# Performance work log

Measured on AMD Instinct MI355X. Metric: run time of the kernel, lower is better.

Reference implementation:

```python
import jax, jax.numpy as jnp
import numpy as np

N, F, H, C, K = 4096, 128, 128, 10, 4  # nodes, feat dim, hidden, classes, num_graphs
EDGE_P = 0.005


def setup_inputs() -> dict:
    key = jax.random.key(0)
    ks = jax.random.split(key, 20)
    feat_matrix = jax.random.normal(ks[0], (N, F), jnp.float32)
    # binary adjacency (dense_to_sparse + GCNConv without edge_weight => weights all 1)
    adj = (jax.random.uniform(ks[1], (N, N, K)) < EDGE_P).astype(jnp.float32)
    adj_matrix = adj * (1.0 - jnp.eye(N, dtype=jnp.float32))[:, :, None]  # no self loops in input
    s = 0.05
    gcn_w1 = jax.random.normal(ks[2], (K, F, H), jnp.float32) * s
    gcn_b1 = jnp.zeros((K, H), jnp.float32)
    gcn_w2 = jax.random.normal(ks[3], (K, H, H), jnp.float32) * s
    gcn_b2 = jnp.zeros((K, H), jnp.float32)
    # PyTorch LSTM params (gate order i,f,g,o), forward and backward directions
    wih_f = jax.random.normal(ks[4], (4 * H, H), jnp.float32) * s
    whh_f = jax.random.normal(ks[5], (4 * H, H), jnp.float32) * s
    bih_f = jnp.zeros((4 * H,), jnp.float32)
    bhh_f = jnp.zeros((4 * H,), jnp.float32)
    wih_b = jax.random.normal(ks[6], (4 * H, H), jnp.float32) * s
    whh_b = jax.random.normal(ks[7], (4 * H, H), jnp.float32) * s
    bih_b = jnp.zeros((4 * H,), jnp.float32)
    bhh_b = jnp.zeros((4 * H,), jnp.float32)
    rnn_out_w = jax.random.normal(ks[8], (1, 2 * H), jnp.float32) * s
    rnn_out_b = jnp.zeros((1,), jnp.float32)
    out_w = jax.random.normal(ks[9], (C, H), jnp.float32) * s
    out_b = jnp.zeros((C,), jnp.float32)
    get_item_index = jnp.arange(N, dtype=jnp.int64)
    set_index = jax.random.randint(ks[10], (1024,), 0, N).astype(jnp.int64)
    val_index = jax.random.randint(ks[11], (1024,), 0, N).astype(jnp.int64)
    mask_matrix = jnp.ones((N,), jnp.bool_)
    return dict(feat_matrix=feat_matrix, adj_matrix=adj_matrix,
                gcn_w1=gcn_w1, gcn_b1=gcn_b1, gcn_w2=gcn_w2, gcn_b2=gcn_b2,
                wih_f=wih_f, whh_f=whh_f, bih_f=bih_f, bhh_f=bhh_f,
                wih_b=wih_b, whh_b=whh_b, bih_b=bih_b, bhh_b=bhh_b,
                rnn_out_w=rnn_out_w, rnn_out_b=rnn_out_b, out_w=out_w, out_b=out_b,
                get_item_index=get_item_index, set_index=set_index,
                val_index=val_index, mask_matrix=mask_matrix)


def _gcn_norm(adj):
    # GCNConv default: A_hat = A + I, sym-normalized D^-1/2 A_hat D^-1/2
    a_hat = adj + jnp.eye(adj.shape[0], dtype=adj.dtype)
    dinv = jax.lax.rsqrt(a_hat.sum(axis=1))
    return dinv[:, None] * a_hat * dinv[None, :]


def _lstm_dir(xs, wih, whh, bih, bhh, reverse):
    # xs: [N, K, H] -> hs: [N, K, H]; scan over the (short) block axis K
    n, h = xs.shape[0], whh.shape[1]
    def step(carry, x_t):
        hp, cp = carry
        g = x_t @ wih.T + hp @ whh.T + (bih + bhh)
        i, f, gg, o = jnp.split(g, 4, axis=-1)
        c = jax.nn.sigmoid(f) * cp + jax.nn.sigmoid(i) * jnp.tanh(gg)
        hn = jax.nn.sigmoid(o) * jnp.tanh(c)
        return (hn, c), hn
    init = (jnp.zeros((n, h), xs.dtype), jnp.zeros((n, h), xs.dtype))
    _, hs = jax.lax.scan(step, init, jnp.swapaxes(xs, 0, 1), reverse=reverse)
    return jnp.swapaxes(hs, 0, 1)


def reference(feat_matrix, adj_matrix, gcn_w1, gcn_b1, gcn_w2, gcn_b2,
              wih_f, whh_f, bih_f, bhh_f, wih_b, whh_b, bih_b, bhh_b,
              rnn_out_w, rnn_out_b, out_w, out_b,
              get_item_index, set_index, val_index, mask_matrix):
    k_blocks = adj_matrix.shape[-1]
    gnn_output = []
    for k in range(k_blocks):  # fixed small number of structurally distinct graph blocks
        an = _gcn_norm(adj_matrix[:, :, k])                 # [N, N]
        h = an @ (feat_matrix @ gcn_w1[k]) + gcn_b1[k]      # GCNConv 1 (no activation)
        h = an @ (h @ gcn_w2[k]) + gcn_b2[k]                # GCNConv 2
        gnn_output.append(h)
    gnn_out = jnp.stack(gnn_output, axis=1)                 # [N, K, H]
    h_fwd = _lstm_dir(gnn_out, wih_f, whh_f, bih_f, bhh_f, reverse=False)
    h_bwd = _lstm_dir(gnn_out, wih_b, whh_b, bih_b, bhh_b, reverse=True)
    rnn_hid = jnp.concatenate([h_fwd, h_bwd], axis=-1)      # [N, K, 2H]
    attn = jax.nn.softmax(rnn_hid @ rnn_out_w.T + rnn_out_b, axis=1)  # [N, K, 1]
    pooled = (gnn_out * attn).sum(axis=1)                   # [N, H]
    return jax.nn.softmax(pooled @ out_w.T + out_b, axis=-1)  # [N, C]
```

## Files before the change

### kernel.cpp

```cpp
#include <hip/hip_runtime.h>
#include <hip/hip_bf16.h>

#define NN 4096
#define HD 128
#define KG 4
#define NC 10
#define CAP 64

typedef __attribute__((ext_vector_type(8))) short bf16x8;
typedef __attribute__((ext_vector_type(4))) float f32x4;

__device__ inline unsigned short f2b(float x) {
    unsigned u = __float_as_uint(x);
    return (unsigned short)((u + 0x7FFFu + ((u >> 16) & 1u)) >> 16);
}
__device__ inline float b2f(unsigned short b) {
    return __uint_as_float((unsigned)b << 16);
}

__global__ __launch_bounds__(256) void setup_kernel(
    const float* __restrict__ adj, const float* __restrict__ feat,
    const float* __restrict__ wih_f, const float* __restrict__ whh_f,
    const float* __restrict__ bih_f, const float* __restrict__ bhh_f,
    const float* __restrict__ wih_b, const float* __restrict__ whh_b,
    const float* __restrict__ bih_b, const float* __restrict__ bhh_b,
    const float* __restrict__ gw1, const float* __restrict__ gw2,
    float* __restrict__ dinv, int* __restrict__ ecnt,
    unsigned short* __restrict__ edges, unsigned* __restrict__ featb,
    unsigned short* __restrict__ Wp, float* __restrict__ bp,
    unsigned short* __restrict__ Wg1p, unsigned short* __restrict__ Wg2p)
{
    int b = blockIdx.x;
    __shared__ int cnt[KG];
    if (b < NN) {
        int i = b;
        int lane = threadIdx.x & 63;
        if (threadIdx.x < KG) cnt[threadIdx.x] = 0;
        __syncthreads();
        const float4* row = (const float4*)(adj + (size_t)i * NN * KG);
        unsigned long long below = (1ull << lane) - 1ull;
        for (int j = threadIdx.x; j < NN; j += 256) {
            float4 v = row[j];
#pragma unroll
            for (int k = 0; k < KG; ++k) {
                float comp = (k == 0) ? v.x : (k == 1) ? v.y : (k == 2) ? v.z : v.w;
                unsigned long long mask = __ballot(comp != 0.f);
                if (mask) {
                    int base;
                    if (lane == 0) base = atomicAdd(&cnt[k], __popcll(mask));
                    base = __shfl(base, 0);
                    if (comp != 0.f) {
                        int p = base + (int)__popcll(mask & below);
                        if (p < CAP)
                            edges[((size_t)(k * NN + i)) * CAP + p] = (unsigned short)j;
                    }
                }
            }
        }
        __syncthreads();
        if (threadIdx.x < KG) {
            int c = cnt[threadIdx.x];
            ecnt[threadIdx.x * NN + i] = c > CAP ? CAP : c;
            dinv[threadIdx.x * NN + i] = rsqrtf((float)c + 1.0f);
        }
    } else if (b < NN + 1024) {
        int t = (b - NN) * 256 + threadIdx.x;
        int dir = t >> 17, rem = t & 131071;
        int n = rem >> 8, k = rem & 255;
        int hq = n >> 6, g = (n >> 4) & 3, hr = n & 15;
        int row = g * HD + hq * 16 + hr;
        const float* wih = dir ? wih_b : wih_f;
        const float* whh = dir ? whh_b : whh_f;
        Wp[t] = f2b(k < HD ? wih[row * HD + k] : whh[row * HD + (k - HD)]);
    } else if (b < NN + 1280) {
        int t = (b - NN - 1024) * 256 + threadIdx.x;
        int n = t >> 7, k = t & 127;
        Wg1p[t] = f2b(gw1[(((size_t)(n >> 7)) * HD + k) * HD + (n & 127)]);
    } else if (b < NN + 1536) {
        int t = (b - NN - 1280) * 256 + threadIdx.x;
        int n = t >> 7, k = t & 127;
        Wg2p[t] = f2b(gw2[(((size_t)(n >> 7)) * HD + k) * HD + (n & 127)]);
    } else if (b < NN + 2560) {
        int t = (b - NN - 1536) * 256 + threadIdx.x;
        float2 v = *(const float2*)&feat[2 * (size_t)t];
        featb[t] = (unsigned)f2b(v.x) | ((unsigned)f2b(v.y) << 16);
    } else {
        int t = (b - NN - 2560) * 256 + threadIdx.x;
        if (t < 1024) {
            int dir = t >> 9, n = t & 511;
            int hq = n >> 6, g = (n >> 4) & 3, hr = n & 15;
            int row = g * HD + hq * 16 + hr;
            bp[t] = dir ? (bih_b[row] + bhh_b[row]) : (bih_f[row] + bhh_f[row]);
        }
    }
}

__global__ __launch_bounds__(256) void gemm_gcn_mfma(
    const unsigned short* __restrict__ Ab, int a_per_k,
    const unsigned short* __restrict__ Bp, const float* __restrict__ dinv,
    unsigned short* __restrict__ Cb)
{
    __shared__ unsigned short Abuf[64 * 40];
    __shared__ unsigned short Bbuf[128 * 40];
    int kg = blockIdx.x, m0 = blockIdx.y * 64;
    const unsigned short* A = Ab + (a_per_k ? (size_t)kg * NN * HD : 0);
    int wid = threadIdx.x >> 6, lane = threadIdx.x & 63;
    int wm = wid >> 1, wn = wid & 1;
    int la = lane & 15, kb = (lane >> 4) * 8;
    f32x4 acc[2][4] = {};
    for (int ch = 0; ch < 4; ++ch) {
        {
            int t = threadIdx.x, r = t >> 2, q = t & 3;
            *(uint4*)&Abuf[r * 40 + q * 8] =
                *(const uint4*)&A[((size_t)(m0 + r)) * HD + ch * 32 + q * 8];
        }
#pragma unroll
        for (int it = 0; it < 2; ++it) {
            int f = threadIdx.x + it * 256;
            int r = f >> 2, q = f & 3;
            *(uint4*)&Bbuf[r * 40 + q * 8] =
                *(const uint4*)&Bp[((size_t)(kg * 128 + r)) * HD + ch * 32 + q * 8];
        }
        __syncthreads();
        bf16x8 a[2], bb[4];
#pragma unroll
        for (int m = 0; m < 2; ++m)
            a[m] = *(const bf16x8*)&Abuf[(wm * 32 + m * 16 + la) * 40 + kb];
#pragma unroll
        for (int n = 0; n < 4; ++n)
            bb[n] = *(const bf16x8*)&Bbuf[(wn * 64 + n * 16 + la) * 40 + kb];
#pragma unroll
        for (int m = 0; m < 2; ++m)
#pragma unroll
            for (int n = 0; n < 4; ++n)
                acc[m][n] = __builtin_amdgcn_mfma_f32_16x16x32_bf16(a[m], bb[n], acc[m][n], 0, 0, 0);
        __syncthreads();
    }
    unsigned short* Ck = Cb + (size_t)kg * NN * HD;
    const float* dv = dinv + kg * NN;
    int lj = lane >> 4;
#pragma unroll
    for (int m = 0; m < 2; ++m)
#pragma unroll
        for (int j = 0; j < 4; ++j) {
            int r = m0 + wm * 32 + m * 16 + lj * 4 + j;
            float d = dv[r];
#pragma unroll
            for (int n = 0; n < 4; ++n) {
                int col = wn * 64 + n * 16 + la;
                Ck[(size_t)r * HD + col] = f2b(acc[m][n][j] * d);
            }
        }
}

__global__ __launch_bounds__(256) void spmm_kernel(
    const unsigned* __restrict__ Zs, const float* __restrict__ dinv,
    const int* __restrict__ ecnt, const unsigned short* __restrict__ edges,
    const float* __restrict__ bias, unsigned* __restrict__ Outb)
{
    int wid = threadIdx.x >> 6, lane = threadIdx.x & 63;
    int idx = blockIdx.x * 4 + wid;
    int k = idx >> 12, i = idx & (NN - 1);
    int cnt = ecnt[idx];
    float di = dinv[idx];
    const unsigned* Zk = Zs + (size_t)k * NN * 64;
    int myj = edges[(size_t)idx * CAP + lane];
    float ax = 0.f, ay = 0.f;
    for (int e = 0; e < cnt; e += 4) {
        int rem = cnt - e;
        int j0 = __shfl(myj, e);
        int j1 = __shfl(myj, e + 1);
        int j2 = __shfl(myj, e + 2);
        int j3 = __shfl(myj, e + 3);
        unsigned z0 = Zk[(size_t)j0 * 64 + lane];
        unsigned z1 = (rem > 1) ? Zk[(size_t)j1 * 64 + lane] : 0u;
        unsigned z2 = (rem > 2) ? Zk[(size_t)j2 * 64 + lane] : 0u;
        unsigned z3 = (rem > 3) ? Zk[(size_t)j3 * 64 + lane] : 0u;
        ax += (b2f((unsigned short)z0) + b2f((unsigned short)z1))
            + (b2f((unsigned short)z2) + b2f((unsigned short)z3));
        ay += (b2f((unsigned short)(z0 >> 16)) + b2f((unsigned short)(z1 >> 16)))
            + (b2f((unsigned short)(z2 >> 16)) + b2f((unsigned short)(z3 >> 16)));
    }
    unsigned zi = Zk[(size_t)i * 64 + lane];
    ax += b2f((unsigned short)zi);
    ay += b2f((unsigned short)(zi >> 16));
    float2 bv = *(const float2*)(bias + k * HD + 2 * lane);
    float ox = fmaf(di, ax, bv.x);
    float oy = fmaf(di, ay, bv.y);
    Outb[(size_t)idx * 64 + lane] = (unsigned)f2b(ox) | ((unsigned)f2b(oy) << 16);
}

__global__ __launch_bounds__(256) void lstm_fused(
    const unsigned short* __restrict__ G2b, unsigned short* __restrict__ hsb,
    const unsigned short* __restrict__ Wp, const float* __restrict__ bp)
{
    __shared__ unsigned short Bbuf[512 * 40];
    __shared__ unsigned short Abuf[64 * 40];
    __shared__ unsigned short hlds[64 * 136];
    int m0 = blockIdx.x * 64;
    int dir = blockIdx.y;
    int wid = threadIdx.x >> 6, lane = threadIdx.x & 63;
    int la = lane & 15, lj = lane >> 4, kb = lj * 8;
    const unsigned short* B = Wp + (size_t)dir * 512 * 256;
    float c_st[4][2][4] = {};
    float bias[2][4];
#pragma unroll
    for (int ch = 0; ch < 2; ++ch)
#pragma unroll
        for (int g = 0; g < 4; ++g)
            bias[ch][g] = bp[dir * 512 + wid * 128 + (ch * 4 + g) * 16 + la];

    for (int t = 0; t < KG; ++t) {
        int kin = dir ? (KG - 1 - t) : t;
        f32x4 acc[4][8] = {};
        int nch = (t == 0) ? 4 : 8;
        for (int ch = 0; ch < nch; ++ch) {
            if (ch < 4) {
                int r = threadIdx.x >> 2, q = threadIdx.x & 3;
                *(uint4*)&Abuf[r * 40 + q * 8] =
                    *(const uint4*)&G2b[((size_t)kin * NN + m0 + r) * HD + ch * 32 + q * 8];
            }
#pragma unroll
            for (int it = 0; it < 8; ++it) {
                int f = threadIdx.x + it * 256;
                int r = f >> 2, q = f & 3;
                *(uint4*)&Bbuf[r * 40 + q * 8] =
                    *(const uint4*)&B[(size_t)r * 256 + ch * 32 + q * 8];
            }
            __syncthreads();
            bf16x8 bfr[8];
#pragma unroll
            for (int fi = 0; fi < 8; ++fi)
                bfr[fi] = *(const bf16x8*)&Bbuf[(wid * 128 + fi * 16 + la) * 40 + kb];
#pragma unroll
            for (int m = 0; m < 4; ++m) {
                bf16x8 afr = (ch < 4)
                    ? *(const bf16x8*)&Abuf[(m * 16 + la) * 40 + kb]
                    : *(const bf16x8*)&hlds[(m * 16 + la) * 136 + (ch - 4) * 32 + kb];
#pragma unroll
                for (int fi = 0; fi < 8; ++fi)
                    acc[m][fi] = __builtin_amdgcn_mfma_f32_16x16x32_bf16(afr, bfr[fi], acc[m][fi], 0, 0, 0);
            }
            __syncthreads();
        }
        unsigned short* hout = hsb + ((size_t)(dir * KG + kin) * NN) * HD;
#pragma unroll
        for (int m = 0; m < 4; ++m)
#pragma unroll
            for (int j = 0; j < 4; ++j) {
                int r = m * 16 + lj * 4 + j;
#pragma unroll
                for (int chf = 0; chf < 2; ++chf) {
                    int h = wid * 32 + chf * 16 + la;
                    float gi = acc[m][chf * 4 + 0][j] + bias[chf][0];
                    float gf = acc[m][chf * 4 + 1][j] + bias[chf][1];
                    float gg = acc[m][chf * 4 + 2][j] + bias[chf][2];
                    float go = acc[m][chf * 4 + 3][j] + bias[chf][3];
                    float cold = c_st[m][chf][j];
                    float si = 1.f / (1.f + __expf(-gi));
                    float sf = 1.f / (1.f + __expf(-gf));
                    float so = 1.f / (1.f + __expf(-go));
                    float e2g = __expf(2.f * gg);
                    float tg = 1.f - 2.f / (e2g + 1.f);
                    float cn = fmaf(sf, cold, si * tg);
                    float e2c = __expf(2.f * cn);
                    float tc = 1.f - 2.f / (e2c + 1.f);
                    c_st[m][chf][j] = cn;
                    unsigned short hb = f2b(so * tc);
                    hlds[r * 136 + h] = hb;
                    hout[(size_t)(m0 + r) * HD + h] = hb;
                }
            }
        __syncthreads();
    }
}

__global__ __launch_bounds__(256) void finalize_kernel(
    const unsigned* __restrict__ gnnb, const unsigned* __restrict__ hsu,
    const float* __restrict__ rw, const float* __restrict__ ow,
    const float* __restrict__ ob, float* __restrict__ out)
{
    int wid = threadIdx.x >> 6, lane = threadIdx.x & 63;
    int n = blockIdx.x * 4 + wid;
    int u0 = 2 * lane;
    float w0 = rw[u0], w1 = rw[u0 + 1];
    float w2 = rw[HD + u0], w3 = rw[HD + u0 + 1];
    float lg[KG];
#pragma unroll
    for (int k = 0; k < KG; ++k) {
        unsigned hf = hsu[((size_t)k * NN + n) * 64 + lane];
        unsigned hb = hsu[((size_t)(KG + k) * NN + n) * 64 + lane];
        lg[k] = b2f((unsigned short)hf) * w0 + b2f((unsigned short)(hf >> 16)) * w1
              + b2f((unsigned short)hb) * w2 + b2f((unsigned short)(hb >> 16)) * w3;
    }
#pragma unroll
    for (int s = 32; s > 0; s >>= 1)
#pragma unroll
        for (int k = 0; k < KG; ++k) lg[k] += __shfl_xor(lg[k], s);
    float mx = lg[0];
#pragma unroll
    for (int k = 1; k < KG; ++k) mx = fmaxf(mx, lg[k]);
    float es[KG], se = 0.f;
#pragma unroll
    for (int k = 0; k < KG; ++k) { es[k] = __expf(lg[k] - mx); se += es[k]; }
    float inv = 1.f / se;
    float p0 = 0.f, p1 = 0.f;
#pragma unroll
    for (int k = 0; k < KG; ++k) {
        float a = es[k] * inv;
        unsigned g = gnnb[((size_t)k * NN + n) * 64 + lane];
        p0 = fmaf(a, b2f((unsigned short)g), p0);
        p1 = fmaf(a, b2f((unsigned short)(g >> 16)), p1);
    }
    float oc[NC];
#pragma unroll
    for (int c = 0; c < NC; ++c)
        oc[c] = p0 * ow[c * HD + u0] + p1 * ow[c * HD + u0 + 1];
#pragma unroll
    for (int s = 32; s > 0; s >>= 1)
#pragma unroll
        for (int c = 0; c < NC; ++c) oc[c] += __shfl_xor(oc[c], s);
    float omx = oc[0] + ob[0];
#pragma unroll
    for (int c = 0; c < NC; ++c) { oc[c] += ob[c]; omx = fmaxf(omx, oc[c]); }
    float osum = 0.f;
#pragma unroll
    for (int c = 0; c < NC; ++c) { oc[c] = __expf(oc[c] - omx); osum += oc[c]; }
    float oinv = 1.f / osum;
    if (lane < NC) out[(size_t)n * NC + lane] = oc[lane] * oinv;
}

extern "C" void kernel_launch(void* const* d_in, const int* in_sizes, int n_in,
                              void* d_out, int out_size, void* d_ws, size_t ws_size,
                              hipStream_t stream)
{
    const float* feat  = (const float*)d_in[0];
    const float* adj   = (const float*)d_in[1];
    const float* gw1   = (const float*)d_in[2];
    const float* gb1   = (const float*)d_in[3];
    const float* gw2   = (const float*)d_in[4];
    const float* gb2   = (const float*)d_in[5];
    const float* wih_f = (const float*)d_in[6];
    const float* whh_f = (const float*)d_in[7];
    const float* bih_f = (const float*)d_in[8];
    const float* bhh_f = (const float*)d_in[9];
    const float* wih_b = (const float*)d_in[10];
    const float* whh_b = (const float*)d_in[11];
    const float* bih_b = (const float*)d_in[12];
    const float* bhh_b = (const float*)d_in[13];
    const float* rw    = (const float*)d_in[14];
    const float* ow    = (const float*)d_in[16];
    const float* ob    = (const float*)d_in[17];
    float* out = (float*)d_out;

    char* ws = (char*)d_ws;
    float*          dinv  = (float*)(ws);
    int*            ecnt  = (int*)(ws + 65536);
    unsigned short* edges = (unsigned short*)(ws + 131072);
    unsigned*       featb = (unsigned*)(ws + 2228224);
    unsigned short* Zs    = (unsigned short*)(ws + 3276800);
    unsigned*       G1b   = (unsigned*)(ws + 7471104);
    unsigned*       G2b   = (unsigned*)(ws + 11665408);
    unsigned short* hsb   = (unsigned short*)(ws + 15859712);
    unsigned short* Wp    = (unsigned short*)(ws + 24248320);
    float*          bp    = (float*)(ws + 24772608);
    unsigned short* Wg1p  = (unsigned short*)(ws + 24776704);
    unsigned short* Wg2p  = (unsigned short*)(ws + 24907776);

    setup_kernel<<<NN + 2564, 256, 0, stream>>>(
        adj, feat, wih_f, whh_f, bih_f, bhh_f, wih_b, whh_b, bih_b, bhh_b,
        gw1, gw2, dinv, ecnt, edges, featb, Wp, bp, Wg1p, Wg2p);
    gemm_gcn_mfma<<<dim3(KG, 64), 256, 0, stream>>>(
        (const unsigned short*)featb, 0, Wg1p, dinv, Zs);
    spmm_kernel<<<KG * NN / 4, 256, 0, stream>>>(
        (const unsigned*)Zs, dinv, ecnt, edges, gb1, G1b);
    gemm_gcn_mfma<<<dim3(KG, 64), 256, 0, stream>>>(
        (const unsigned short*)G1b, 1, Wg2p, dinv, Zs);
    spmm_kernel<<<KG * NN / 4, 256, 0, stream>>>(
        (const unsigned*)Zs, dinv, ecnt, edges, gb2, G2b);
    lstm_fused<<<dim3(64, 2), 256, 0, stream>>>(
        (const unsigned short*)G2b, hsb, Wp, bp);
    finalize_kernel<<<NN / 4, 256, 0, stream>>>(
        G2b, (const unsigned*)hsb, rw, ow, ob, out);
}
```

Before: 499.3 us.

## Fuse first GCN SpMM with second-layer dense GEMM via LDS staging

The first sparse aggregation and the second GCN weight GEMM now run in one kernel. Each 512-thread block aggregates 64 rows into LDS, then applies MFMA against the second-layer weights, so the intermediate G1 never goes through global memory and one launch disappears. In exchange the grid shrinks from 4096 blocks to 256, which cuts parallelism for the latency-bound gather phase. Each wave also handles 8 rows one after another.

```diff
diff --git a/kernel.cpp b/kernel.cpp
--- a/kernel.cpp
+++ b/kernel.cpp
@@ -96,14 +96,14 @@
 }
 
 __global__ __launch_bounds__(256) void gemm_gcn_mfma(
-    const unsigned short* __restrict__ Ab, int a_per_k,
+    const unsigned short* __restrict__ Ab,
     const unsigned short* __restrict__ Bp, const float* __restrict__ dinv,
     unsigned short* __restrict__ Cb)
 {
     __shared__ unsigned short Abuf[64 * 40];
     __shared__ unsigned short Bbuf[128 * 40];
     int kg = blockIdx.x, m0 = blockIdx.y * 64;
-    const unsigned short* A = Ab + (a_per_k ? (size_t)kg * NN * HD : 0);
+    const unsigned short* A = Ab;
     int wid = threadIdx.x >> 6, lane = threadIdx.x & 63;
     int wm = wid >> 1, wn = wid & 1;
     int la = lane & 15, kb = (lane >> 4) * 8;
@@ -151,6 +151,82 @@
                 Ck[(size_t)r * HD + col] = f2b(acc[m][n][j] * d);
             }
         }
+}
+
+__global__ __launch_bounds__(512) void spmm_gemm_fused(
+    const unsigned* __restrict__ Zs, const float* __restrict__ dinv,
+    const int* __restrict__ ecnt, const unsigned short* __restrict__ edges,
+    const float* __restrict__ bias, const unsigned short* __restrict__ Bp,
+    unsigned short* __restrict__ Cb)
+{
+    __shared__ unsigned short Alds[64 * 136];
+    __shared__ unsigned short Bbuf[128 * 40];
+    int kg = blockIdx.x, m0 = blockIdx.y * 64;
+    int wid = threadIdx.x >> 6, lane = threadIdx.x & 63;
+    const unsigned* Zk = Zs + (size_t)kg * NN * 64;
+    for (int rr = 0; rr < 8; ++rr) {
+        int r = wid * 8 + rr;
+        int i = m0 + r;
+        int idx = (kg << 12) + i;
+        int cnt = ecnt[idx];
+        float di = dinv[idx];
+        int myj = edges[(size_t)idx * CAP + lane];
+        float ax = 0.f, ay = 0.f;
+        for (int e = 0; e < cnt; e += 4) {
+            int rem = cnt - e;
+            int j0 = __shfl(myj, e);
+            int j1 = __shfl(myj, e + 1);
+            int j2 = __shfl(myj, e + 2);
+            int j3 = __shfl(myj, e + 3);
+            unsigned z0 = Zk[(size_t)j0 * 64 + lane];
+            unsigned z1 = (rem > 1) ? Zk[(size_t)j1 * 64 + lane] : 0u;
+            unsigned z2 = (rem > 2) ? Zk[(size_t)j2 * 64 + lane] : 0u;
+            unsigned z3 = (rem > 3) ? Zk[(size_t)j3 * 64 + lane] : 0u;
+            ax += (b2f((unsigned short)z0) + b2f((unsigned short)z1))
+                + (b2f((unsigned short)z2) + b2f((unsigned short)z3));
+            ay += (b2f((unsigned short)(z0 >> 16)) + b2f((unsigned short)(z1 >> 16)))
+                + (b2f((unsigned short)(z2 >> 16)) + b2f((unsigned short)(z3 >> 16)));
+        }
+        unsigned zi = Zk[(size_t)i * 64 + lane];
+        ax += b2f((unsigned short)zi);
+        ay += b2f((unsigned short)(zi >> 16));
+        float2 bv = *(const float2*)(bias + kg * HD + 2 * lane);
+        float ox = fmaf(di, ax, bv.x);
+        float oy = fmaf(di, ay, bv.y);
+        ((unsigned*)Alds)[r * 68 + lane] = (unsigned)f2b(ox) | ((unsigned)f2b(oy) << 16);
+    }
+    __syncthreads();
+    int wm = wid >> 1, wn = wid & 1;
+    int la = lane & 15, kb = (lane >> 4) * 8;
+    f32x4 acc[4] = {};
+    for (int ch = 0; ch < 4; ++ch) {
+        {
+            int rb = threadIdx.x >> 2, q = threadIdx.x & 3;
+            *(uint4*)&Bbuf[rb * 40 + q * 8] =
+                *(const uint4*)&Bp[((size_t)(kg * 128 + rb)) * HD + ch * 32 + q * 8];
+        }
+        __syncthreads();
+        bf16x8 a = *(const bf16x8*)&Alds[(wm * 16 + la) * 136 + ch * 32 + kb];
+#pragma unroll
+        for (int n = 0; n < 4; ++n) {
+            bf16x8 bb = *(const bf16x8*)&Bbuf[(wn * 64 + n * 16 + la) * 40 + kb];
+            acc[n] = __builtin_amdgcn_mfma_f32_16x16x32_bf16(a, bb, acc[n], 0, 0, 0);
+        }
+        __syncthreads();
+    }
+    unsigned short* Ck = Cb + (size_t)kg * NN * HD;
+    const float* dv = dinv + kg * NN;
+    int lj = lane >> 4;
+#pragma unroll
+    for (int j = 0; j < 4; ++j) {
+        int r = m0 + wm * 16 + lj * 4 + j;
+        float d = dv[r];
+#pragma unroll
+        for (int n = 0; n < 4; ++n) {
+            int col = wn * 64 + n * 16 + la;
+            Ck[(size_t)r * HD + col] = f2b(acc[n][j] * d);
+        }
+    }
 }
 
 __global__ __launch_bounds__(256) void spmm_kernel(
@@ -359,7 +435,7 @@
     unsigned short* edges = (unsigned short*)(ws + 131072);
     unsigned*       featb = (unsigned*)(ws + 2228224);
     unsigned short* Zs    = (unsigned short*)(ws + 3276800);
-    unsigned*       G1b   = (unsigned*)(ws + 7471104);
+    unsigned short* Zs2   = (unsigned short*)(ws + 7471104);
     unsigned*       G2b   = (unsigned*)(ws + 11665408);
     unsigned short* hsb   = (unsigned short*)(ws + 15859712);
     unsigned short* Wp    = (unsigned short*)(ws + 24248320);
@@ -371,13 +447,11 @@
         adj, feat, wih_f, whh_f, bih_f, bhh_f, wih_b, whh_b, bih_b, bhh_b,
         gw1, gw2, dinv, ecnt, edges, featb, Wp, bp, Wg1p, Wg2p);
     gemm_gcn_mfma<<<dim3(KG, 64), 256, 0, stream>>>(
-        (const unsigned short*)featb, 0, Wg1p, dinv, Zs);
+        (const unsigned short*)featb, Wg1p, dinv, Zs);
+    spmm_gemm_fused<<<dim3(KG, 64), 512, 0, stream>>>(
+        (const unsigned*)Zs, dinv, ecnt, edges, gb1, Wg2p, Zs2);
     spmm_kernel<<<KG * NN / 4, 256, 0, stream>>>(
-        (const unsigned*)Zs, dinv, ecnt, edges, gb1, G1b);
-    gemm_gcn_mfma<<<dim3(KG, 64), 256, 0, stream>>>(
-        (const unsigned short*)G1b, 1, Wg2p, dinv, Zs);
-    spmm_kernel<<<KG * NN / 4, 256, 0, stream>>>(
-        (const unsigned*)Zs, dinv, ecnt, edges, gb2, G2b);
+        (const unsigned*)Zs2, dinv, ecnt, edges, gb2, G2b);
     lstm_fused<<<dim3(64, 2), 256, 0, stream>>>(
         (const unsigned short*)G2b, hsb, Wp, bp);
     finalize_kernel<<<NN / 4, 256, 0, stream>>>(
```

Measured after the change: 510.8 us. +2.3%, slower.
